# Performance work log

Hardware: AMD Instinct MI355X
Metric: run time of the kernel (lower is better)

## Reference

```python
import jax, jax.numpy as jnp
import numpy as np

N, H, W = 2, 96, 96
HL, WL = 48, 48
NCLS = 59


def _bn_params(key, c):
    k1, k2, k3, k4 = jax.random.split(key, 4)
    g = jax.random.uniform(k1, (c,), minval=0.5, maxval=1.5)
    b = jax.random.normal(k2, (c,)) * 0.1
    m = jax.random.normal(k3, (c,)) * 0.1
    v = jax.random.uniform(k4, (c,), minval=0.5, maxval=1.5)
    return jnp.stack([g, b, m, v])  # [4, C]


def _conv_w(key, shape):
    fan_in = shape[1] * shape[2] * shape[3]
    return jax.random.normal(key, shape) / np.sqrt(fan_in)


def setup_inputs() -> dict:
    key = jax.random.key(0)
    ks = jax.random.split(key, 32)
    return {
        "c1": jax.random.normal(ks[0], (N, 256, H, W)),
        "c2": jax.random.normal(ks[1], (N, 512, HL, WL)),
        "x": jax.random.normal(ks[2], (N, 2048, HL, WL)),
        "w_r1": _conv_w(ks[3], (64, 256, 3, 3)), "bn_r1": _bn_params(ks[4], 64),
        "w_r2": _conv_w(ks[5], (64, 64, 3, 3)), "bn_r2": _bn_params(ks[6], 64),
        "w_r3": _conv_w(ks[7], (64, 512, 1, 1)), "bn_r3": _bn_params(ks[8], 64),
        "w_p1": _conv_w(ks[9], (512, 2048, 1, 1)), "bn_p1": _bn_params(ks[10], 512),
        "w_p2": _conv_w(ks[11], (512, 2048, 1, 1)), "bn_p2": _bn_params(ks[12], 512),
        "w_p3": _conv_w(ks[13], (512, 2048, 1, 1)), "bn_p3": _bn_params(ks[14], 512),
        "w_p4": _conv_w(ks[15], (512, 2048, 1, 1)), "bn_p4": _bn_params(ks[16], 512),
        "w_c5": _conv_w(ks[17], (512, 4096, 3, 3)), "bn_c5": _bn_params(ks[18], 512),
        "w_c6": _conv_w(ks[19], (NCLS, 512, 1, 1)),
        "b_c6": jax.random.normal(ks[20], (NCLS,)) * 0.01,
    }


def conv2d(x, w, padding=0, dilation=1):
    return jax.lax.conv_general_dilated(
        x, w, window_strides=(1, 1), padding=[(padding, padding)] * 2,
        rhs_dilation=(dilation, dilation),
        dimension_numbers=("NCHW", "OIHW", "NCHW"))


def bn(x, p, eps=1e-5):
    g, b, m, v = p[0], p[1], p[2], p[3]
    scale = g * jax.lax.rsqrt(v + eps)
    return (x - m[None, :, None, None]) * scale[None, :, None, None] + b[None, :, None, None]


def resize_bilinear_ac(x, oh, ow):
    # bilinear, align_corners=True (matches torch interpolate)
    n, c, h, w = x.shape
    def coords(inp, out):
        if inp == 1 or out == 1:
            return jnp.zeros((out,), jnp.float32)
        return jnp.arange(out, dtype=jnp.float32) * ((inp - 1) / (out - 1))
    ys, xs = coords(h, oh), coords(w, ow)
    y0 = jnp.clip(jnp.floor(ys).astype(jnp.int32), 0, h - 1)
    y1 = jnp.clip(y0 + 1, 0, h - 1)
    wy = (ys - y0)[None, None, :, None]
    x0 = jnp.clip(jnp.floor(xs).astype(jnp.int32), 0, w - 1)
    x1 = jnp.clip(x0 + 1, 0, w - 1)
    wx = (xs - x0)[None, None, :]
    g = x[:, :, y0, :] * (1.0 - wy) + x[:, :, y1, :] * wy  # [n,c,oh,w]
    return g[:, :, :, x0] * (1.0 - wx[:, None]) + g[:, :, :, x1] * wx[:, None]


def unfold3x3_d2(x):
    # torch unfold(kernel=3, dilation=2, padding=2, stride=1) -> [n,c,9,h*w]
    n, c, h, w = x.shape
    p = jnp.pad(x, ((0, 0), (0, 0), (2, 2), (2, 2)))
    pats = jnp.stack([p[:, :, dy:dy + h, dx:dx + w]
                      for dy in (0, 2, 4) for dx in (0, 2, 4)], axis=2)
    return pats.reshape(n, c, 9, h * w)


def adaptive_avg_pool(x, s):
    n, c, h, w = x.shape  # h, w divisible by s here
    return x.reshape(n, c, s, h // s, s, w // s).mean(axis=(3, 5))


def reference(c1, c2, x, w_r1, bn_r1, w_r2, bn_r2, w_r3, bn_r3,
              w_p1, bn_p1, w_p2, bn_p2, w_p3, bn_p3, w_p4, bn_p4,
              w_c5, bn_c5, w_c6, b_c6):
    n, _, h, w = c1.shape
    # refine(c1): two dilated 3x3 convs -> query features [n,64,h,w]
    r = jax.nn.relu(bn(conv2d(c1, w_r1, padding=2, dilation=2), bn_r1))
    r = jax.nn.relu(bn(conv2d(r, w_r2, padding=2, dilation=2), bn_r2))
    # c2 -> upsample -> refine2 (1x1) -> key features [n,64,h,w]
    c2u = resize_bilinear_ac(c2, h, w)
    c2r = jax.nn.relu(bn(conv2d(c2u, w_r3), bn_r3))
    uc2 = unfold3x3_d2(c2r)                       # [n,64,9,hw]
    q = r.reshape(n, 64, h * w)                   # [n,64,hw]
    energy = jnp.einsum("ncp,nckp->npk", q, uc2)  # [n,hw,9]
    att = jax.nn.softmax(energy, axis=-1)
    # conv5 = PyramidPooling + 3x3 conv(4096->512) + BN + ReLU
    xh, xw = x.shape[2], x.shape[3]
    feats = [x]
    for s, wp, bnp in ((1, w_p1, bn_p1), (2, w_p2, bn_p2), (3, w_p3, bn_p3), (6, w_p4, bn_p4)):
        p = jax.nn.relu(bn(conv2d(adaptive_avg_pool(x, s), wp), bnp))
        feats.append(resize_bilinear_ac(p, xh, xw))
    psp = jnp.concatenate(feats, axis=1)          # [n,4096,xh,xw]
    out = jax.nn.relu(bn(conv2d(psp, w_c5, padding=1, dilation=1), bn_c5))  # [n,512,xh,xw]
    out0 = resize_bilinear_ac(out, h, w)          # [n,512,h,w]
    uo = unfold3x3_d2(out0)                       # [n,512,9,hw]
    agg = jnp.einsum("npk,nckp->ncp", att, uo).reshape(n, 512, h, w)
    # conv6: Dropout2d in eval mode = identity, then 1x1 conv with bias
    return conv2d(agg, w_c6) + b_c6[None, :, None, None]
```

## Files before the change

kernel.cpp:

```cpp
#include <hip/hip_runtime.h>
#include <hip/hip_bf16.h>
#include <cstddef>
#include <cstdint>

typedef __hip_bfloat16 hbf;
typedef __bf16 bf16x8 __attribute__((ext_vector_type(8)));
typedef float f32x4 __attribute__((ext_vector_type(4)));

#define GLDS(gp, lp) __builtin_amdgcn_global_load_lds( \
    (const __attribute__((address_space(1))) void*)(gp), \
    (__attribute__((address_space(3))) void*)(lp), 16, 0, 0)

__device__ __forceinline__ void bn_coef(const float* __restrict__ p, int C, int c,
                                        float& s, float& t) {
    float g = p[c];
    float b = p[C + c];
    float m = p[2 * C + c];
    float v = p[3 * C + c];
    s = g * rsqrtf(v + 1e-5f);
    t = b - m * s;
}

__global__ void k_fill0(uint32_t* __restrict__ p, int n) {
    int i = blockIdx.x * blockDim.x + threadIdx.x;
    if (i < n) p[i] = 0u;
}

__global__ __launch_bounds__(256) void k_c1trans(const float* __restrict__ x,
                                                 hbf* __restrict__ c1t) {
    __shared__ float tbuf[32][33];
    const int p0 = blockIdx.x * 32, c0 = blockIdx.y * 32, n = blockIdx.z;
    const int tx = threadIdx.x, ty = threadIdx.y;
#pragma unroll
    for (int i = 0; i < 4; ++i) {
        int ci = c0 + ty * 4 + i;
        tbuf[ty * 4 + i][tx] = x[((size_t)(n * 256 + ci)) * 9216 + p0 + tx];
    }
    __syncthreads();
#pragma unroll
    for (int i = 0; i < 4; ++i) {
        int p = p0 + ty * 4 + i;
        int pp = (p / 96 + 2) * 100 + (p % 96) + 2;
        c1t[((size_t)(n * 10000 + pp)) * 256 + c0 + tx] = __float2bfloat16(tbuf[tx][ty * 4 + i]);
    }
}

template <int CI>
__global__ __launch_bounds__(256) void k_wtrans_small(const float* __restrict__ w,
                                                      hbf* __restrict__ wt) {
    int idx = blockIdx.x * 256 + threadIdx.x;
    int co = idx / CI, ci = idx % CI;
    const float* s = w + ((size_t)(co * CI + ci)) * 9;
#pragma unroll
    for (int tap = 0; tap < 9; ++tap)
        wt[((size_t)(tap * 64 + co)) * CI + ci] = __float2bfloat16(s[tap]);
}

template <int CI>
__global__ __launch_bounds__(256) void k_dconv_mfma(const hbf* __restrict__ wt,
                                                    const hbf* __restrict__ it,
                                                    float* __restrict__ accout) {
    __shared__ hbf As[2][3][64 * 32];
    __shared__ hbf Bs[2][72 * 32];
    const int tid = threadIdx.x;
    const int l = tid & 63, w = tid >> 6;
    const int P0 = blockIdx.x * 64;
    const int g  = blockIdx.y;
    const int r0 = tid >> 2;
    const int swzk = ((tid & 3) ^ ((r0 >> 1) & 3)) * 8;

    const int n_i = P0 / 9216;
    const int pl0 = P0 - n_i * 9216;
    const int pp0 = (pl0 / 96 + 2) * 100 + (pl0 % 96) + 2;
    const ptrdiff_t browbase = (ptrdiff_t)n_i * 10000 + pp0 + (g - 1) * 200 - 2;

    const int wn = w * 16;
    const int pl_lane = pl0 + wn + (l & 15);
    const int jb = ((pl_lane / 96 + 2) * 100 + (pl_lane % 96) + 2) - pp0;
    const int slotA = ((l >> 4) ^ ((l >> 1) & 3)) * 8;

    f32x4 acc[4];
#pragma unroll
    for (int i = 0; i < 4; ++i) acc[i] = {0.f, 0.f, 0.f, 0.f};

    const hbf* gA = wt + ((size_t)(g * 192 + r0)) * CI + swzk;
    const hbf* gB = it + (size_t)(browbase + r0) * CI + swzk;

#define STAGE_D(buf, k0) do {                                                  \
        hbf* ldsA_ = &As[buf][0][0] + w * 512;                                 \
        hbf* ldsB_ = &Bs[buf][0] + w * 512;                                    \
        _Pragma("unroll")                                                      \
        for (int t_ = 0; t_ < 3; ++t_)                                         \
            GLDS(gA + (size_t)t_ * 64 * CI + (k0), ldsA_ + t_ * 2048);         \
        GLDS(gB + (k0), ldsB_);                                                \
        if (tid < 32)                                                          \
            GLDS(gB + (size_t)64 * CI + (k0), &Bs[buf][0] + 2048);             \
    } while (0)

    STAGE_D(0, 0);
    int cur = 0;
#pragma unroll 2
    for (int k0 = 0; k0 < CI; k0 += 32) {
        __syncthreads();
        if (k0 + 32 < CI) STAGE_D(cur ^ 1, k0 + 32);
        __builtin_amdgcn_s_setprio(1);
#pragma unroll
        for (int t = 0; t < 3; ++t) {
            const int brow = jb + 2 * t;
            bf16x8 bfr = *(const bf16x8*)(&Bs[cur][0] + brow * 32 + (((l >> 4) ^ ((brow >> 1) & 3)) * 8));
#pragma unroll
            for (int ti = 0; ti < 4; ++ti) {
                bf16x8 af = *(const bf16x8*)(&As[cur][t][(ti * 16 + (l & 15)) * 32 + slotA]);
                acc[ti] = __builtin_amdgcn_mfma_f32_16x16x32_bf16(af, bfr, acc[ti], 0, 0, 0);
            }
        }
        __builtin_amdgcn_s_setprio(0);
        cur ^= 1;
    }
#undef STAGE_D

    const int px = P0 + wn + (l & 15);
    const int n2 = px / 9216, pl2 = px % 9216;
#pragma unroll
    for (int ti = 0; ti < 4; ++ti) {
        const int mrow = ti * 16 + (l >> 4) * 4;
        float* dst = accout + ((size_t)(n2 * 64 + mrow)) * 9216 + pl2;
#pragma unroll
        for (int r = 0; r < 4; ++r)
            atomicAdd(dst + (size_t)r * 9216, acc[ti][r]);
    }
}

__global__ __launch_bounds__(256) void k_ep_r1(const float* __restrict__ acc,
                                               const float* __restrict__ bnp,
                                               hbf* __restrict__ r1t) {
    __shared__ float ss[64], st[64];
    if (threadIdx.x < 64) {
        float s, t; bn_coef(bnp, 64, threadIdx.x, s, t);
        ss[threadIdx.x] = s; st[threadIdx.x] = t;
    }
    __syncthreads();
    const int pi = blockIdx.x * 256 + threadIdx.x;
    const int n = pi / 9216, pl = pi % 9216;
    const int pp = (pl / 96 + 2) * 100 + (pl % 96) + 2;
    hbf* dst = r1t + ((size_t)(n * 10000 + pp)) * 64;
    const float* src = acc + (size_t)n * 64 * 9216 + pl;
#pragma unroll
    for (int co = 0; co < 64; ++co)
        dst[co] = __float2bfloat16(fmaxf(fmaf(src[(size_t)co * 9216], ss[co], st[co]), 0.f));
}

__global__ __launch_bounds__(192) void k_conv1x1_c2(const float* __restrict__ c2,
                                                    const float* __restrict__ w,
                                                    float* __restrict__ outacc) {
    const int x = threadIdx.x;
    const int y = blockIdx.y * 4 + threadIdx.y;
    const int n = blockIdx.z >> 2;
    const int ci0 = (blockIdx.z & 3) * 128;
    const int cg = blockIdx.x;
    const int p = y * 48 + x;
    float acc[8];
#pragma unroll
    for (int j = 0; j < 8; ++j) acc[j] = 0.f;
    for (int ci = ci0; ci < ci0 + 128; ++ci) {
        float iv = c2[(size_t)(n * 512 + ci) * 2304 + p];
#pragma unroll
        for (int j = 0; j < 8; ++j)
            acc[j] = fmaf(iv, w[(size_t)(cg * 8 + j) * 512 + ci], acc[j]);
    }
#pragma unroll
    for (int j = 0; j < 8; ++j)
        atomicAdd(&outacc[(size_t)(n * 64 + cg * 8 + j) * 2304 + p], acc[j]);
}

__global__ void k_up96(const float* __restrict__ src, float* __restrict__ dst,
                       int C, const float* __restrict__ bnp) {
    int idx = blockIdx.x * blockDim.x + threadIdx.x;
    int p = idx % 9216;
    int nc = idx / 9216;
    int c = nc % C;
    int y = p / 96, x = p % 96;
    int yn = y * 47, xn = x * 47;
    int y0 = yn / 95, x0 = xn / 95;
    float wy = (float)(yn - y0 * 95) * (1.f / 95.f);
    float wx = (float)(xn - x0 * 95) * (1.f / 95.f);
    int y1 = min(y0 + 1, 47), x1 = min(x0 + 1, 47);
    const float* sp = src + (size_t)nc * 2304;
    float v00 = sp[y0 * 48 + x0], v01 = sp[y0 * 48 + x1];
    float v10 = sp[y1 * 48 + x0], v11 = sp[y1 * 48 + x1];
    float v = (v00 * (1.f - wx) + v01 * wx) * (1.f - wy)
            + (v10 * (1.f - wx) + v11 * wx) * wy;
    if (bnp) {
        float s, t; bn_coef(bnp, C, c, s, t);
        v = fmaxf(fmaf(v, s, t), 0.f);
    }
    dst[idx] = v;
}

__global__ __launch_bounds__(256) void k_attention(const float* __restrict__ qa,
                                                   const float* __restrict__ bnp,
                                                   const float* __restrict__ kf,
                                                   float* __restrict__ att) {
    const int wv = threadIdx.x >> 6;
    const int ln = threadIdx.x & 63;
    const int p_abs = blockIdx.x * 64 + ln;
    const int n = p_abs / 9216, p = p_abs % 9216;
    const int y = p / 96, x = p % 96;
    const float* qb = qa + ((size_t)(n * 64 + wv * 16)) * 9216 + p;
    float qv[16];
#pragma unroll
    for (int c = 0; c < 16; ++c) {
        float s, t; bn_coef(bnp, 64, wv * 16 + c, s, t);
        qv[c] = fmaxf(fmaf(qb[(size_t)c * 9216], s, t), 0.f);
    }
    const float* kb = kf + ((size_t)(n * 64 + wv * 16)) * 9216;
    float e[9];
#pragma unroll
    for (int ky = 0; ky < 3; ++ky)
#pragma unroll
        for (int kx = 0; kx < 3; ++kx) {
            int yy = y + 2 * ky - 2, xx = x + 2 * kx - 2;
            float s = 0.f;
            if (yy >= 0 && yy < 96 && xx >= 0 && xx < 96) {
                const float* kp = kb + yy * 96 + xx;
#pragma unroll
                for (int c = 0; c < 16; ++c) s = fmaf(qv[c], kp[(size_t)c * 9216], s);
            }
            e[ky * 3 + kx] = s;
        }
    __shared__ float pe[9][4][64];
#pragma unroll
    for (int k = 0; k < 9; ++k) pe[k][wv][ln] = e[k];
    __syncthreads();
    if (threadIdx.x < 64) {
        float ee[9];
#pragma unroll
        for (int k = 0; k < 9; ++k)
            ee[k] = (pe[k][0][ln] + pe[k][1][ln]) + (pe[k][2][ln] + pe[k][3][ln]);
        float m = ee[0];
#pragma unroll
        for (int k = 1; k < 9; ++k) m = fmaxf(m, ee[k]);
        float sum = 0.f;
#pragma unroll
        for (int k = 0; k < 9; ++k) { ee[k] = __expf(ee[k] - m); sum += ee[k]; }
        float inv = 1.f / sum;
        float* ap = att + (size_t)p_abs * 9;
#pragma unroll
        for (int k = 0; k < 9; ++k) ap[k] = ee[k] * inv;
    }
}

__global__ __launch_bounds__(64) void k_pool(const float* __restrict__ xin,
                                             float* __restrict__ pooled) {
    int b = blockIdx.x;
    int t = threadIdx.x;
    __shared__ float cells[50];
    if (t < 50) cells[t] = 0.f;
    __syncthreads();
    float rs = 0.f;
    if (t < 48) {
        const float* row = xin + (size_t)b * 2304 + t * 48;
        float s6[6];
#pragma unroll
        for (int j = 0; j < 6; ++j) {
            float s = 0.f;
#pragma unroll
            for (int i = 0; i < 8; ++i) s += row[j * 8 + i];
            s6[j] = s;
        }
        float s3a = s6[0] + s6[1], s3b = s6[2] + s6[3], s3c = s6[4] + s6[5];
        float s2a = s3a + s6[2], s2b = s6[3] + s3c;
        rs = s2a + s2b;
        int r6 = t >> 3, r3 = t >> 4, r2 = t / 24;
        atomicAdd(&cells[14 + r6 * 6 + 0], s6[0]);
        atomicAdd(&cells[14 + r6 * 6 + 1], s6[1]);
        atomicAdd(&cells[14 + r6 * 6 + 2], s6[2]);
        atomicAdd(&cells[14 + r6 * 6 + 3], s6[3]);
        atomicAdd(&cells[14 + r6 * 6 + 4], s6[4]);
        atomicAdd(&cells[14 + r6 * 6 + 5], s6[5]);
        atomicAdd(&cells[5 + r3 * 3 + 0], s3a);
        atomicAdd(&cells[5 + r3 * 3 + 1], s3b);
        atomicAdd(&cells[5 + r3 * 3 + 2], s3c);
        atomicAdd(&cells[1 + r2 * 2 + 0], s2a);
        atomicAdd(&cells[1 + r2 * 2 + 1], s2b);
    }
#pragma unroll
    for (int off = 32; off > 0; off >>= 1) rs += __shfl_down(rs, off);
    if (t == 0) atomicAdd(&cells[0], rs);
    __syncthreads();
    if (t < 50) {
        float inv = (t == 0) ? (1.f / 2304.f)
                  : (t < 5)  ? (1.f / 576.f)
                  : (t < 14) ? (1.f / 256.f)
                             : (1.f / 64.f);
        pooled[(size_t)b * 50 + t] = cells[t] * inv;
    }
}

__global__ __launch_bounds__(64) void k_pconv2(const float* __restrict__ pooled,
        const float* __restrict__ wp1, const float* __restrict__ bn1,
        const float* __restrict__ wp2, const float* __restrict__ bn2,
        const float* __restrict__ wp3, const float* __restrict__ bn3,
        const float* __restrict__ wp4, const float* __restrict__ bn4,
        float* __restrict__ pconv) {
    const int co = blockIdx.x, n = blockIdx.y;
    const int t = threadIdx.x;
    const int cell = (t < 50) ? t : 49;
    const float* w; const float* bnp;
    if (cell == 0)      { w = wp1; bnp = bn1; }
    else if (cell < 5)  { w = wp2; bnp = bn2; }
    else if (cell < 14) { w = wp3; bnp = bn3; }
    else                { w = wp4; bnp = bn4; }
    const float* pin = pooled + (size_t)n * 2048 * 50 + cell;
    const float* wr = w + (size_t)co * 2048;
    float a0 = 0.f, a1 = 0.f, a2 = 0.f, a3 = 0.f;
    for (int c = 0; c < 2048; c += 4) {
        a0 = fmaf(pin[(size_t)c * 50],       wr[c],     a0);
        a1 = fmaf(pin[(size_t)(c + 1) * 50], wr[c + 1], a1);
        a2 = fmaf(pin[(size_t)(c + 2) * 50], wr[c + 2], a2);
        a3 = fmaf(pin[(size_t)(c + 3) * 50], wr[c + 3], a3);
    }
    float a = (a0 + a1) + (a2 + a3);
    float s, tt; bn_coef(bnp, 512, co, s, tt);
    if (t < 50)
        pconv[((size_t)n * 512 + co) * 50 + cell] = fmaxf(fmaf(a, s, tt), 0.f);
}

__global__ __launch_bounds__(256) void k_wpsp_trans(const float* __restrict__ w5,
                                                    hbf* __restrict__ wpsp) {
    const int co = blockIdx.x * 64 + (threadIdx.x & 63);
    const int b = blockIdx.y;
    const int c0 = blockIdx.z * 64 + (threadIdx.x >> 6) * 16;
    for (int i = 0; i < 16; ++i) {
        int c = c0 + i;
        const float* s = w5 + ((size_t)co * 4096 + 2048 + b * 512 + c) * 9;
#pragma unroll
        for (int tap = 0; tap < 9; ++tap)
            wpsp[(((size_t)(tap * 4 + b) * 512) + c) * 512 + co] = __float2bfloat16(s[tap]);
    }
}

__global__ __launch_bounds__(64) void k_computeM2(const hbf* __restrict__ wpsp,
                                                  const float* __restrict__ pconv,
                                                  float* __restrict__ M) {
    const int cog = blockIdx.x, tap = blockIdx.y;
    const int n = blockIdx.z / 7, chunk = blockIdx.z % 7;
    const int cell0_t[7] = {0, 1, 5, 14, 23, 32, 41};
    const int ncell_t[7] = {1, 4, 9, 9, 9, 9, 9};
    const int btab[7]    = {0, 1, 2, 3, 3, 3, 3};
    const int cell0 = cell0_t[chunk], nc = ncell_t[chunk], b = btab[chunk];
    const int co = cog * 64 + threadIdx.x;
    const hbf* wb = wpsp + ((size_t)(tap * 4 + b) * 512) * 512 + co;
    const float* pc = pconv + (size_t)n * 512 * 50 + cell0;
    float acc[9];
#pragma unroll
    for (int j = 0; j < 9; ++j) acc[j] = 0.f;
    for (int c = 0; c < 512; ++c) {
        float w = __bfloat162float(wb[(size_t)c * 512]);
#pragma unroll
        for (int j = 0; j < 9; ++j)
            acc[j] = fmaf(w, pc[c * 50 + j], acc[j]);
    }
    float* Mp = M + ((size_t)(n * 512 + co) * 9 + tap) * 50 + cell0;
    for (int j = 0; j < nc; ++j) Mp[j] = acc[j];
}

struct B4 { int c0, c1, c2, c3; float w0, w1, w2, w3; };
__device__ __forceinline__ B4 cell_interp(int yy, int xx, int s, int base) {
    int sm1 = s - 1;
    int yn = yy * sm1, xn = xx * sm1;
    int y0 = yn / 47, x0 = xn / 47;
    float wy = (float)(yn - y0 * 47) * (1.f / 47.f);
    float wx = (float)(xn - x0 * 47) * (1.f / 47.f);
    int y1 = min(y0 + 1, sm1), x1 = min(x0 + 1, sm1);
    B4 r;
    r.c0 = base + y0 * s + x0; r.c1 = base + y0 * s + x1;
    r.c2 = base + y1 * s + x0; r.c3 = base + y1 * s + x1;
    r.w0 = (1.f - wy) * (1.f - wx); r.w1 = (1.f - wy) * wx;
    r.w2 = wy * (1.f - wx);         r.w3 = wy * wx;
    return r;
}

__global__ __launch_bounds__(256) void k_xtrans(const float* __restrict__ x,
                                                hbf* __restrict__ xtp) {
    __shared__ float tbuf[32][33];
    const int p0 = blockIdx.x * 32, c0 = blockIdx.y * 32, n = blockIdx.z;
    const int tx = threadIdx.x, ty = threadIdx.y;
#pragma unroll
    for (int i = 0; i < 4; ++i) {
        int ci = c0 + ty * 4 + i;
        tbuf[ty * 4 + i][tx] = x[((size_t)(n * 2048 + ci)) * 2304 + p0 + tx];
    }
    __syncthreads();
#pragma unroll
    for (int i = 0; i < 4; ++i) {
        int p = p0 + ty * 4 + i;
        int pp = (p / 48 + 1) * 50 + (p % 48) + 1;
        xtp[((size_t)(n * 2500 + pp)) * 2048 + c0 + tx] = __float2bfloat16(tbuf[tx][ty * 4 + i]);
    }
}

__global__ __launch_bounds__(256) void k_wtrans(const float* __restrict__ w5,
                                                hbf* __restrict__ wt) {
    int idx = blockIdx.x * 256 + threadIdx.x;
    int co = idx >> 11, ci = idx & 2047;
    const float* s = w5 + ((size_t)co * 4096 + ci) * 9;
#pragma unroll
    for (int tap = 0; tap < 9; ++tap)
        wt[((size_t)(tap * 512 + co)) * 2048 + ci] = __float2bfloat16(s[tap]);
}

__global__ __launch_bounds__(256) void k_conv5_mfma(const hbf* __restrict__ wt,
                                                    const hbf* __restrict__ xtp,
                                                    float* __restrict__ c5acc) {
    __shared__ hbf As[2][3][128 * 32];
    __shared__ hbf Bs[2][136 * 32];
    const int tid = threadIdx.x;
    const int l = tid & 63, w = tid >> 6;
    const int m0 = blockIdx.x * 128;
    const int P0 = blockIdx.y * 128;
    const int g  = blockIdx.z;
    const int n_img = P0 / 2304;
    const int pbase = P0 - n_img * 2304;
    const int r0 = tid >> 2;
    const int swzk = ((tid & 3) ^ ((r0 >> 1) & 3)) * 8;

    const int pp0 = pbase + 2 * (pbase / 48) + 51;
    const ptrdiff_t browbase = (ptrdiff_t)n_img * 2500 + pp0 + (g - 1) * 50 - 1;

    const int wm = (w & 1) * 64, wn = (w >> 1) * 64;
    int jb[4];
#pragma unroll
    for (int tj = 0; tj < 4; ++tj) {
        int p = pbase + wn + tj * 16 + (l & 15);
        jb[tj] = p + 2 * (p / 48) + 51 - pp0;
    }
    const int slotA = ((l >> 4) ^ ((l >> 1) & 3)) * 8;

    f32x4 acc[4][4];
#pragma unroll
    for (int i = 0; i < 4; ++i)
#pragma unroll
        for (int j = 0; j < 4; ++j) acc[i][j] = {0.f, 0.f, 0.f, 0.f};

    const hbf* gA = wt + ((size_t)(g * 1536 + m0 + r0)) * 2048 + swzk;
    const hbf* gB = xtp + (size_t)(browbase + r0) * 2048 + swzk;

#define STAGE5(buf, k0) do {                                                       \
        hbf* ldsA_ = &As[buf][0][0] + w * 512;                                     \
        hbf* ldsB_ = &Bs[buf][0] + w * 512;                                        \
        _Pragma("unroll")                                                          \
        for (int t_ = 0; t_ < 3; ++t_) {                                           \
            GLDS(gA + (size_t)t_ * 512 * 2048 + (k0),             ldsA_ + t_ * 4096);      \
            GLDS(gA + (size_t)t_ * 512 * 2048 + 64 * 2048 + (k0), ldsA_ + t_ * 4096 + 2048); \
        }                                                                          \
        GLDS(gB + (k0),                      ldsB_);                               \
        GLDS(gB + (size_t)64 * 2048 + (k0),  ldsB_ + 2048);                        \
        if (tid < 32)                                                              \
            GLDS(gB + (size_t)128 * 2048 + (k0), &Bs[buf][0] + 4096);              \
    } while (0)

    STAGE5(0, 0);
    int cur = 0;
#pragma unroll 2
    for (int k0 = 0; k0 < 2048; k0 += 32) {
        __syncthreads();
        if (k0 + 32 < 2048) STAGE5(cur ^ 1, k0 + 32);
        __builtin_amdgcn_s_setprio(1);
#pragma unroll
        for (int t = 0; t < 3; ++t) {
            bf16x8 af[4], bfr[4];
#pragma unroll
            for (int ti = 0; ti < 4; ++ti)
                af[ti] = *(const bf16x8*)(&As[cur][t][(wm + ti * 16 + (l & 15)) * 32 + slotA]);
#pragma unroll
            for (int tj = 0; tj < 4; ++tj) {
                const int brow = jb[tj] + t;
                bfr[tj] = *(const bf16x8*)(&Bs[cur][0] + brow * 32 + (((l >> 4) ^ ((brow >> 1) & 3)) * 8));
            }
#pragma unroll
            for (int ti = 0; ti < 4; ++ti)
#pragma unroll
                for (int tj = 0; tj < 4; ++tj)
                    acc[ti][tj] = __builtin_amdgcn_mfma_f32_16x16x32_bf16(
                        af[ti], bfr[tj], acc[ti][tj], 0, 0, 0);
        }
        __builtin_amdgcn_s_setprio(0);
        cur ^= 1;
    }
#undef STAGE5

#pragma unroll
    for (int ti = 0; ti < 4; ++ti) {
        const int mrow = wm + ti * 16 + (l >> 4) * 4;
#pragma unroll
        for (int tj = 0; tj < 4; ++tj) {
            const int p = pbase + wn + tj * 16 + (l & 15);
            float* dst = c5acc + ((size_t)(n_img * 512 + m0 + mrow)) * 2304 + p;
#pragma unroll
            for (int r = 0; r < 4; ++r)
                atomicAdd(dst + (size_t)r * 2304, acc[ti][tj][r]);
        }
    }
}

__global__ __launch_bounds__(256) void k_bnrelu_psp(const float* __restrict__ c5acc,
                                                    const float* __restrict__ M,
                                                    const float* __restrict__ bnp,
                                                    hbf* __restrict__ c5out) {
    const int co = blockIdx.x, n = blockIdx.y;
    __shared__ float Ms[450];
    const float* Mrow = M + ((size_t)(n * 512 + co)) * 450;
    for (int i = threadIdx.x; i < 450; i += 256) Ms[i] = Mrow[i];
    __syncthreads();
    float s, t; bn_coef(bnp, 512, co, s, t);
    const size_t base = ((size_t)(n * 512 + co)) * 2304;
#pragma unroll
    for (int i = 0; i < 9; ++i) {
        int p = threadIdx.x + i * 256;
        int y = p / 48, x = p % 48;
        float a = c5acc[base + p];
#pragma unroll
        for (int ky = 0; ky < 3; ++ky) {
            int yy = y + ky - 1;
            if (yy < 0 || yy > 47) continue;
#pragma unroll
            for (int kx = 0; kx < 3; ++kx) {
                int xx = x + kx - 1;
                if (xx < 0 || xx > 47) continue;
                const float* Mp = Ms + (ky * 3 + kx) * 50;
                float sa = Mp[0];
                B4 b2 = cell_interp(yy, xx, 2, 1);
                B4 b3 = cell_interp(yy, xx, 3, 5);
                B4 b6 = cell_interp(yy, xx, 6, 14);
                sa = fmaf(b2.w0, Mp[b2.c0], sa); sa = fmaf(b2.w1, Mp[b2.c1], sa);
                sa = fmaf(b2.w2, Mp[b2.c2], sa); sa = fmaf(b2.w3, Mp[b2.c3], sa);
                sa = fmaf(b3.w0, Mp[b3.c0], sa); sa = fmaf(b3.w1, Mp[b3.c1], sa);
                sa = fmaf(b3.w2, Mp[b3.c2], sa); sa = fmaf(b3.w3, Mp[b3.c3], sa);
                sa = fmaf(b6.w0, Mp[b6.c0], sa); sa = fmaf(b6.w1, Mp[b6.c1], sa);
                sa = fmaf(b6.w2, Mp[b6.c2], sa); sa = fmaf(b6.w3, Mp[b6.c3], sa);
                a += sa;
            }
        }
        c5out[base + p] = __float2bfloat16(fmaxf(fmaf(a, s, t), 0.f));
    }
}

__global__ __launch_bounds__(192) void k_conv6s(const hbf* __restrict__ c5o,
                                                const float* __restrict__ w,
                                                float* __restrict__ out) {
    const int x = threadIdx.x;
    const int y = blockIdx.y * 4 + threadIdx.y;
    const int n = blockIdx.z;
    const int co = blockIdx.x;
    const int p = y * 48 + x;
    const hbf* ip = c5o + (size_t)n * 512 * 2304 + p;
    const float* wr = w + (size_t)co * 512;
    float a0 = 0.f, a1 = 0.f, a2 = 0.f, a3 = 0.f;
    for (int ci = 0; ci < 512; ci += 4) {
        a0 = fmaf(__bfloat162float(ip[(size_t)ci * 2304]),       wr[ci],     a0);
        a1 = fmaf(__bfloat162float(ip[(size_t)(ci + 1) * 2304]), wr[ci + 1], a1);
        a2 = fmaf(__bfloat162float(ip[(size_t)(ci + 2) * 2304]), wr[ci + 2], a2);
        a3 = fmaf(__bfloat162float(ip[(size_t)(ci + 3) * 2304]), wr[ci + 3], a3);
    }
    out[((size_t)n * 59 + co) * 2304 + p] = (a0 + a1) + (a2 + a3);
}

__global__ void k_final(const float* __restrict__ att, const float* __restrict__ c6o,
                        const float* __restrict__ bias, float* __restrict__ out) {
    int idx = blockIdx.x * blockDim.x + threadIdx.x;
    int p = idx % 9216;
    int nc = idx / 9216;
    int cls = nc % 59, n = nc / 59;
    int y = p / 96, x = p % 96;
    const float* ar = att + ((size_t)n * 9216 + p) * 9;
    const float* cp = c6o + (size_t)nc * 9216;
    float a = bias[cls];
#pragma unroll
    for (int ky = 0; ky < 3; ++ky)
#pragma unroll
        for (int kx = 0; kx < 3; ++kx) {
            int yy = y + 2 * ky - 2, xx = x + 2 * kx - 2;
            if (yy >= 0 && yy < 96 && xx >= 0 && xx < 96)
                a = fmaf(ar[ky * 3 + kx], cp[yy * 96 + xx], a);
        }
    out[idx] = a;
}

extern "C" void kernel_launch(void* const* d_in, const int* in_sizes, int n_in,
                              void* d_out, int out_size, void* d_ws, size_t ws_size,
                              hipStream_t stream) {
    const float* c1    = (const float*)d_in[0];
    const float* c2    = (const float*)d_in[1];
    const float* xin   = (const float*)d_in[2];
    const float* w_r1  = (const float*)d_in[3];
    const float* bn_r1 = (const float*)d_in[4];
    const float* w_r2  = (const float*)d_in[5];
    const float* bn_r2 = (const float*)d_in[6];
    const float* w_r3  = (const float*)d_in[7];
    const float* bn_r3 = (const float*)d_in[8];
    const float* w_p1  = (const float*)d_in[9];
    const float* bn_p1 = (const float*)d_in[10];
    const float* w_p2  = (const float*)d_in[11];
    const float* bn_p2 = (const float*)d_in[12];
    const float* w_p3  = (const float*)d_in[13];
    const float* bn_p3 = (const float*)d_in[14];
    const float* w_p4  = (const float*)d_in[15];
    const float* bn_p4 = (const float*)d_in[16];
    const float* w_c5  = (const float*)d_in[17];
    const float* bn_c5 = (const float*)d_in[18];
    const float* w_c6  = (const float*)d_in[19];
    const float* b_c6  = (const float*)d_in[20];
    float* out = (float*)d_out;
    (void)in_sizes; (void)n_in; (void)out_size; (void)ws_size;

    char* base = (char*)d_ws;
    float* att = (float*)base;
    char*  A   = base + 663552;
    hbf*   c1t   = (hbf*)A;
    hbf*   r1t   = (hbf*)(A + 10240000);
    float* r1acc = (float*)(A + 12800000);
    float* qacc  = (float*)(A + 17518592);
    float* c2acc = (float*)(A + 22237184);
    float* q     = (float*)(A + 23416832);
    float* c2r   = (float*)(A + 28135424);
    hbf*   wr1t  = (hbf*)(A + 32854016);
    hbf*   wr2t  = (hbf*)(A + 33148928);
    hbf*   wpsp   = (hbf*)A;
    float* pooled = (float*)(A + 48791552);
    float* pconv  = (float*)(A + 49610752);
    float* M      = (float*)(A + 49815552);
    hbf*   xtp    = (hbf*)A;
    float* c5acc  = (float*)(A + 20480000);
    hbf*   wt     = (hbf*)(A + 29917184);
    hbf*   c5out = (hbf*)A;
    float* c6s   = (float*)(A + 4718592);
    float* c6o   = (float*)(A + 5806080);
    (void)q;

    k_fill0<<<dim3(22868), 256, 0, stream>>>((uint32_t*)A, 5854208);
    k_c1trans<<<dim3(288, 8, 2), dim3(32, 8), 0, stream>>>(c1, c1t);
    k_wtrans_small<256><<<dim3(64), 256, 0, stream>>>(w_r1, wr1t);
    k_wtrans_small<64><<<dim3(16), 256, 0, stream>>>(w_r2, wr2t);
    k_dconv_mfma<256><<<dim3(288, 3), 256, 0, stream>>>(wr1t, c1t, r1acc);
    k_ep_r1<<<dim3(72), 256, 0, stream>>>(r1acc, bn_r1, r1t);
    k_dconv_mfma<64><<<dim3(288, 3), 256, 0, stream>>>(wr2t, r1t, qacc);
    k_conv1x1_c2<<<dim3(8, 12, 8), dim3(48, 4), 0, stream>>>(c2, w_r3, c2acc);
    k_up96<<<dim3(2 * 64 * 9216 / 256), 256, 0, stream>>>(c2acc, c2r, 64, bn_r3);
    k_attention<<<dim3(288), 256, 0, stream>>>(qacc, bn_r2, c2r, att);
    k_pool<<<dim3(4096), 64, 0, stream>>>(xin, pooled);
    k_pconv2<<<dim3(512, 2), 64, 0, stream>>>(pooled, w_p1, bn_p1, w_p2, bn_p2,
                                              w_p3, bn_p3, w_p4, bn_p4, pconv);
    k_wpsp_trans<<<dim3(8, 4, 8), 256, 0, stream>>>(w_c5, wpsp);
    k_computeM2<<<dim3(8, 9, 14), 64, 0, stream>>>(wpsp, pconv, M);
    k_fill0<<<dim3(29216), 256, 0, stream>>>((uint32_t*)xtp, 7479296);
    k_xtrans<<<dim3(72, 64, 2), dim3(32, 8), 0, stream>>>(xin, xtp);
    k_wtrans<<<dim3(4096), 256, 0, stream>>>(w_c5, wt);
    k_conv5_mfma<<<dim3(4, 36, 3), 256, 0, stream>>>(wt, xtp, c5acc);
    k_bnrelu_psp<<<dim3(512, 2), 256, 0, stream>>>(c5acc, M, bn_c5, c5out);
    k_conv6s<<<dim3(59, 12, 2), dim3(48, 4), 0, stream>>>(c5out, w_c6, c6s);
    k_up96<<<dim3(2 * 59 * 9216 / 256), 256, 0, stream>>>(c6s, c6o, 59, nullptr);
    k_final<<<dim3(2 * 59 * 9216 / 256), 256, 0, stream>>>(att, c6o, b_c6, out);
}
```

Baseline: 652.4 us.

## Fuse weight transposes, fold final upsample into aggregation, vectorize small kernels

Merges the two small weight-transpose kernels and the two conv5 weight-transpose kernels into single launches, removing launch gaps. Drops the separate bilinear upsample of the conv6 output and instead interpolates on the fly from the 48x48 map inside the final attention-aggregation kernel, avoiding a full-resolution intermediate. Also vectorizes conv6s loads and stores (4 pixels per thread with bf16x4), vectorizes pool row sums, spreads the r1 epilogue across more blocks, and removes setprio from the dconv loop. The fused final kernel recomputes interpolation per tap, which adds arithmetic and gathers, and the interpolation ordering differs slightly in floating point.

```diff
diff --git a/kernel.cpp b/kernel.cpp
--- a/kernel.cpp
+++ b/kernel.cpp
@@ -5,6 +5,7 @@
 
 typedef __hip_bfloat16 hbf;
 typedef __bf16 bf16x8 __attribute__((ext_vector_type(8)));
+typedef __bf16 bf16x4 __attribute__((ext_vector_type(4)));
 typedef float f32x4 __attribute__((ext_vector_type(4)));
 
 #define GLDS(gp, lp) __builtin_amdgcn_global_load_lds( \
@@ -45,15 +46,26 @@
     }
 }
 
-template <int CI>
-__global__ __launch_bounds__(256) void k_wtrans_small(const float* __restrict__ w,
-                                                      hbf* __restrict__ wt) {
-    int idx = blockIdx.x * 256 + threadIdx.x;
-    int co = idx / CI, ci = idx % CI;
-    const float* s = w + ((size_t)(co * CI + ci)) * 9;
-#pragma unroll
-    for (int tap = 0; tap < 9; ++tap)
-        wt[((size_t)(tap * 64 + co)) * CI + ci] = __float2bfloat16(s[tap]);
+__global__ __launch_bounds__(256) void k_wsmall(const float* __restrict__ w1,
+                                                hbf* __restrict__ wt1,
+                                                const float* __restrict__ w2,
+                                                hbf* __restrict__ wt2) {
+    int b = blockIdx.x;
+    if (b < 64) {
+        int idx = b * 256 + threadIdx.x;
+        int co = idx >> 8, ci = idx & 255;
+        const float* s = w1 + ((size_t)(co * 256 + ci)) * 9;
+#pragma unroll
+        for (int tap = 0; tap < 9; ++tap)
+            wt1[((size_t)(tap * 64 + co)) * 256 + ci] = __float2bfloat16(s[tap]);
+    } else {
+        int idx = (b - 64) * 256 + threadIdx.x;
+        int co = idx >> 6, ci = idx & 63;
+        const float* s = w2 + ((size_t)(co * 64 + ci)) * 9;
+#pragma unroll
+        for (int tap = 0; tap < 9; ++tap)
+            wt2[((size_t)(tap * 64 + co)) * 64 + ci] = __float2bfloat16(s[tap]);
+    }
 }
 
 template <int CI>
@@ -103,7 +115,6 @@
     for (int k0 = 0; k0 < CI; k0 += 32) {
         __syncthreads();
         if (k0 + 32 < CI) STAGE_D(cur ^ 1, k0 + 32);
-        __builtin_amdgcn_s_setprio(1);
 #pragma unroll
         for (int t = 0; t < 3; ++t) {
             const int brow = jb + 2 * t;
@@ -114,7 +125,6 @@
                 acc[ti] = __builtin_amdgcn_mfma_f32_16x16x32_bf16(af, bfr, acc[ti], 0, 0, 0);
             }
         }
-        __builtin_amdgcn_s_setprio(0);
         cur ^= 1;
     }
 #undef STAGE_D
@@ -134,20 +144,18 @@
 __global__ __launch_bounds__(256) void k_ep_r1(const float* __restrict__ acc,
                                                const float* __restrict__ bnp,
                                                hbf* __restrict__ r1t) {
-    __shared__ float ss[64], st[64];
-    if (threadIdx.x < 64) {
-        float s, t; bn_coef(bnp, 64, threadIdx.x, s, t);
-        ss[threadIdx.x] = s; st[threadIdx.x] = t;
-    }
-    __syncthreads();
-    const int pi = blockIdx.x * 256 + threadIdx.x;
+    const int q = threadIdx.x >> 6;
+    const int ln = threadIdx.x & 63;
+    const int pi = blockIdx.x * 64 + ln;
     const int n = pi / 9216, pl = pi % 9216;
     const int pp = (pl / 96 + 2) * 100 + (pl % 96) + 2;
-    hbf* dst = r1t + ((size_t)(n * 10000 + pp)) * 64;
-    const float* src = acc + (size_t)n * 64 * 9216 + pl;
-#pragma unroll
-    for (int co = 0; co < 64; ++co)
-        dst[co] = __float2bfloat16(fmaxf(fmaf(src[(size_t)co * 9216], ss[co], st[co]), 0.f));
+    hbf* dst = r1t + ((size_t)(n * 10000 + pp)) * 64 + q * 16;
+    const float* src = acc + (size_t)(n * 64 + q * 16) * 9216 + pl;
+#pragma unroll
+    for (int i = 0; i < 16; ++i) {
+        float s, t; bn_coef(bnp, 64, q * 16 + i, s, t);
+        dst[i] = __float2bfloat16(fmaxf(fmaf(src[(size_t)i * 9216], s, t), 0.f));
+    }
 }
 
 __global__ __launch_bounds__(192) void k_conv1x1_c2(const float* __restrict__ c2,
@@ -259,14 +267,12 @@
     __syncthreads();
     float rs = 0.f;
     if (t < 48) {
-        const float* row = xin + (size_t)b * 2304 + t * 48;
+        const f32x4* rowv = (const f32x4*)(xin + (size_t)b * 2304 + t * 48);
         float s6[6];
 #pragma unroll
         for (int j = 0; j < 6; ++j) {
-            float s = 0.f;
-#pragma unroll
-            for (int i = 0; i < 8; ++i) s += row[j * 8 + i];
-            s6[j] = s;
+            f32x4 u = rowv[2 * j], v = rowv[2 * j + 1];
+            s6[j] = ((u[0] + u[1]) + (u[2] + u[3])) + ((v[0] + v[1]) + (v[2] + v[3]));
         }
         float s3a = s6[0] + s6[1], s3b = s6[2] + s6[3], s3c = s6[4] + s6[5];
         float s2a = s3a + s6[2], s2b = s6[3] + s3c;
@@ -326,17 +332,29 @@
         pconv[((size_t)n * 512 + co) * 50 + cell] = fmaxf(fmaf(a, s, tt), 0.f);
 }
 
-__global__ __launch_bounds__(256) void k_wpsp_trans(const float* __restrict__ w5,
+__global__ __launch_bounds__(256) void k_wtrans_all(const float* __restrict__ w5,
+                                                    hbf* __restrict__ wt,
                                                     hbf* __restrict__ wpsp) {
-    const int co = blockIdx.x * 64 + (threadIdx.x & 63);
-    const int b = blockIdx.y;
-    const int c0 = blockIdx.z * 64 + (threadIdx.x >> 6) * 16;
-    for (int i = 0; i < 16; ++i) {
-        int c = c0 + i;
-        const float* s = w5 + ((size_t)co * 4096 + 2048 + b * 512 + c) * 9;
+    int b = blockIdx.x;
+    if (b < 4096) {
+        int idx = b * 256 + threadIdx.x;
+        int co = idx >> 11, ci = idx & 2047;
+        const float* s = w5 + ((size_t)co * 4096 + ci) * 9;
 #pragma unroll
         for (int tap = 0; tap < 9; ++tap)
-            wpsp[(((size_t)(tap * 4 + b) * 512) + c) * 512 + co] = __float2bfloat16(s[tap]);
+            wt[((size_t)(tap * 512 + co)) * 2048 + ci] = __float2bfloat16(s[tap]);
+    } else {
+        int r = b - 4096;
+        const int co = (r & 7) * 64 + (threadIdx.x & 63);
+        const int bb = (r >> 3) & 3;
+        const int c0 = (r >> 5) * 64 + (threadIdx.x >> 6) * 16;
+        for (int i = 0; i < 16; ++i) {
+            int c = c0 + i;
+            const float* s = w5 + ((size_t)co * 4096 + 2048 + bb * 512 + c) * 9;
+#pragma unroll
+            for (int tap = 0; tap < 9; ++tap)
+                wpsp[(((size_t)(tap * 4 + bb) * 512) + c) * 512 + co] = __float2bfloat16(s[tap]);
+        }
     }
 }
 
@@ -398,16 +416,6 @@
         int pp = (p / 48 + 1) * 50 + (p % 48) + 1;
         xtp[((size_t)(n * 2500 + pp)) * 2048 + c0 + tx] = __float2bfloat16(tbuf[tx][ty * 4 + i]);
     }
-}
-
-__global__ __launch_bounds__(256) void k_wtrans(const float* __restrict__ w5,
-                                                hbf* __restrict__ wt) {
-    int idx = blockIdx.x * 256 + threadIdx.x;
-    int co = idx >> 11, ci = idx & 2047;
-    const float* s = w5 + ((size_t)co * 4096 + ci) * 9;
-#pragma unroll
-    for (int tap = 0; tap < 9; ++tap)
-        wt[((size_t)(tap * 512 + co)) * 2048 + ci] = __float2bfloat16(s[tap]);
 }
 
 __global__ __launch_bounds__(256) void k_conv5_mfma(const hbf* __restrict__ wt,
@@ -549,24 +557,25 @@
 __global__ __launch_bounds__(192) void k_conv6s(const hbf* __restrict__ c5o,
                                                 const float* __restrict__ w,
                                                 float* __restrict__ out) {
-    const int x = threadIdx.x;
-    const int y = blockIdx.y * 4 + threadIdx.y;
+    const int p4 = blockIdx.y * 192 + threadIdx.x;
     const int n = blockIdx.z;
     const int co = blockIdx.x;
-    const int p = y * 48 + x;
-    const hbf* ip = c5o + (size_t)n * 512 * 2304 + p;
+    const hbf* ip = c5o + (size_t)n * 512 * 2304 + p4 * 4;
     const float* wr = w + (size_t)co * 512;
     float a0 = 0.f, a1 = 0.f, a2 = 0.f, a3 = 0.f;
-    for (int ci = 0; ci < 512; ci += 4) {
-        a0 = fmaf(__bfloat162float(ip[(size_t)ci * 2304]),       wr[ci],     a0);
-        a1 = fmaf(__bfloat162float(ip[(size_t)(ci + 1) * 2304]), wr[ci + 1], a1);
-        a2 = fmaf(__bfloat162float(ip[(size_t)(ci + 2) * 2304]), wr[ci + 2], a2);
-        a3 = fmaf(__bfloat162float(ip[(size_t)(ci + 3) * 2304]), wr[ci + 3], a3);
-    }
-    out[((size_t)n * 59 + co) * 2304 + p] = (a0 + a1) + (a2 + a3);
-}
-
-__global__ void k_final(const float* __restrict__ att, const float* __restrict__ c6o,
+    for (int ci = 0; ci < 512; ++ci) {
+        bf16x4 v = *(const bf16x4*)(ip + (size_t)ci * 2304);
+        float wv = wr[ci];
+        a0 = fmaf((float)v[0], wv, a0);
+        a1 = fmaf((float)v[1], wv, a1);
+        a2 = fmaf((float)v[2], wv, a2);
+        a3 = fmaf((float)v[3], wv, a3);
+    }
+    f32x4 res = {a0, a1, a2, a3};
+    *(f32x4*)(out + ((size_t)n * 59 + co) * 2304 + p4 * 4) = res;
+}
+
+__global__ void k_final(const float* __restrict__ att, const float* __restrict__ c6s,
                         const float* __restrict__ bias, float* __restrict__ out) {
     int idx = blockIdx.x * blockDim.x + threadIdx.x;
     int p = idx % 9216;
@@ -574,16 +583,40 @@
     int cls = nc % 59, n = nc / 59;
     int y = p / 96, x = p % 96;
     const float* ar = att + ((size_t)n * 9216 + p) * 9;
-    const float* cp = c6o + (size_t)nc * 9216;
+    const float* cp = c6s + (size_t)nc * 2304;
+    int xs0[3], xs1[3], ys0[3], ys1[3];
+    float fx[3], fy[3];
+#pragma unroll
+    for (int d = 0; d < 3; ++d) {
+        int xx = x + 2 * d - 2;
+        if (xx >= 0 && xx < 96) {
+            int xn = xx * 47, x0 = xn / 95;
+            xs0[d] = x0; xs1[d] = min(x0 + 1, 47);
+            fx[d] = (float)(xn - x0 * 95) * (1.f / 95.f);
+        } else { xs0[d] = -1; xs1[d] = 0; fx[d] = 0.f; }
+        int yy = y + 2 * d - 2;
+        if (yy >= 0 && yy < 96) {
+            int yn = yy * 47, y0 = yn / 95;
+            ys0[d] = y0; ys1[d] = min(y0 + 1, 47);
+            fy[d] = (float)(yn - y0 * 95) * (1.f / 95.f);
+        } else { ys0[d] = -1; ys1[d] = 0; fy[d] = 0.f; }
+    }
     float a = bias[cls];
 #pragma unroll
-    for (int ky = 0; ky < 3; ++ky)
+    for (int ky = 0; ky < 3; ++ky) {
+        if (ys0[ky] < 0) continue;
+        const float* r0 = cp + ys0[ky] * 48;
+        const float* r1 = cp + ys1[ky] * 48;
+        float wy = fy[ky];
 #pragma unroll
         for (int kx = 0; kx < 3; ++kx) {
-            int yy = y + 2 * ky - 2, xx = x + 2 * kx - 2;
-            if (yy >= 0 && yy < 96 && xx >= 0 && xx < 96)
-                a = fmaf(ar[ky * 3 + kx], cp[yy * 96 + xx], a);
-        }
+            if (xs0[kx] < 0) continue;
+            float wx = fx[kx];
+            float v0 = r0[xs0[kx]] * (1.f - wx) + r0[xs1[kx]] * wx;
+            float v1 = r1[xs0[kx]] * (1.f - wx) + r1[xs1[kx]] * wx;
+            a = fmaf(ar[ky * 3 + kx], v0 * (1.f - wy) + v1 * wy, a);
+        }
+    }
     out[idx] = a;
 }
 
@@ -622,7 +655,6 @@
     float* r1acc = (float*)(A + 12800000);
     float* qacc  = (float*)(A + 17518592);
     float* c2acc = (float*)(A + 22237184);
-    float* q     = (float*)(A + 23416832);
     float* c2r   = (float*)(A + 28135424);
     hbf*   wr1t  = (hbf*)(A + 32854016);
     hbf*   wr2t  = (hbf*)(A + 33148928);
@@ -635,15 +667,12 @@
     hbf*   wt     = (hbf*)(A + 29917184);
     hbf*   c5out = (hbf*)A;
     float* c6s   = (float*)(A + 4718592);
-    float* c6o   = (float*)(A + 5806080);
-    (void)q;
 
     k_fill0<<<dim3(22868), 256, 0, stream>>>((uint32_t*)A, 5854208);
     k_c1trans<<<dim3(288, 8, 2), dim3(32, 8), 0, stream>>>(c1, c1t);
-    k_wtrans_small<256><<<dim3(64), 256, 0, stream>>>(w_r1, wr1t);
-    k_wtrans_small<64><<<dim3(16), 256, 0, stream>>>(w_r2, wr2t);
+    k_wsmall<<<dim3(80), 256, 0, stream>>>(w_r1, wr1t, w_r2, wr2t);
     k_dconv_mfma<256><<<dim3(288, 3), 256, 0, stream>>>(wr1t, c1t, r1acc);
-    k_ep_r1<<<dim3(72), 256, 0, stream>>>(r1acc, bn_r1, r1t);
+    k_ep_r1<<<dim3(288), 256, 0, stream>>>(r1acc, bn_r1, r1t);
     k_dconv_mfma<64><<<dim3(288, 3), 256, 0, stream>>>(wr2t, r1t, qacc);
     k_conv1x1_c2<<<dim3(8, 12, 8), dim3(48, 4), 0, stream>>>(c2, w_r3, c2acc);
     k_up96<<<dim3(2 * 64 * 9216 / 256), 256, 0, stream>>>(c2acc, c2r, 64, bn_r3);
@@ -651,14 +680,12 @@
     k_pool<<<dim3(4096), 64, 0, stream>>>(xin, pooled);
     k_pconv2<<<dim3(512, 2), 64, 0, stream>>>(pooled, w_p1, bn_p1, w_p2, bn_p2,
                                               w_p3, bn_p3, w_p4, bn_p4, pconv);
-    k_wpsp_trans<<<dim3(8, 4, 8), 256, 0, stream>>>(w_c5, wpsp);
+    k_wtrans_all<<<dim3(4352), 256, 0, stream>>>(w_c5, wt, wpsp);
     k_computeM2<<<dim3(8, 9, 14), 64, 0, stream>>>(wpsp, pconv, M);
     k_fill0<<<dim3(29216), 256, 0, stream>>>((uint32_t*)xtp, 7479296);
     k_xtrans<<<dim3(72, 64, 2), dim3(32, 8), 0, stream>>>(xin, xtp);
-    k_wtrans<<<dim3(4096), 256, 0, stream>>>(w_c5, wt);
     k_conv5_mfma<<<dim3(4, 36, 3), 256, 0, stream>>>(wt, xtp, c5acc);
     k_bnrelu_psp<<<dim3(512, 2), 256, 0, stream>>>(c5acc, M, bn_c5, c5out);
-    k_conv6s<<<dim3(59, 12, 2), dim3(48, 4), 0, stream>>>(c5out, w_c6, c6s);
-    k_up96<<<dim3(2 * 59 * 9216 / 256), 256, 0, stream>>>(c6s, c6o, 59, nullptr);
-    k_final<<<dim3(2 * 59 * 9216 / 256), 256, 0, stream>>>(att, c6o, b_c6, out);
-}
+    k_conv6s<<<dim3(59, 3, 2), 192, 0, stream>>>(c5out, w_c6, c6s);
+    k_final<<<dim3(2 * 59 * 9216 / 256), 256, 0, stream>>>(att, c6s, b_c6, out);
+}
```

Result: slower. 684.5 us (+4.9%).
